# Performance work log

Hardware: AMD Instinct MI355X
Metric: run time of the kernel (lower is better)

The kernel has to match this reference:

```python
import jax, jax.numpy as jnp
import numpy as np

B, T, I, H, O = 64, 2048, 128, 256, 1

def setup_inputs() -> dict:
    key = jax.random.key(0)
    ks = jax.random.split(key, 7)
    s = 0.05
    return {
        "x": jax.random.normal(ks[0], (B, T, I), jnp.float32),
        "W_ih": jax.random.normal(ks[1], (3 * H, I), jnp.float32) * s,
        "W_hh": jax.random.normal(ks[2], (3 * H, H), jnp.float32) * s,
        "b_ih": jax.random.normal(ks[3], (3 * H,), jnp.float32) * s,
        "b_hh": jax.random.normal(ks[4], (3 * H,), jnp.float32) * s,
        "W_o": jax.random.normal(ks[5], (O, H), jnp.float32) * s,
        "b_o": jax.random.normal(ks[6], (O,), jnp.float32) * s,
    }

def _gru_scan(x, W_ih, W_hh, b_ih, b_hh):
    # Precompute input projections for all timesteps: [T, B, 3H]
    gi = jnp.einsum('bti,gi->tbg', x, W_ih) + b_ih
    Hd = W_hh.shape[1]

    def step(h, gi_t):
        gh = h @ W_hh.T + b_hh  # [B, 3H]
        i_r, i_z, i_n = jnp.split(gi_t, 3, axis=-1)
        h_r, h_z, h_n = jnp.split(gh, 3, axis=-1)
        r = jax.nn.sigmoid(i_r + h_r)
        z = jax.nn.sigmoid(i_z + h_z)
        n = jnp.tanh(i_n + r * h_n)
        h_new = (1.0 - z) * n + z * h
        return h_new, h_new

    h0 = jnp.zeros((x.shape[0], Hd), x.dtype)
    _, hs = jax.lax.scan(step, h0, gi)  # hs: [T, B, H]
    return hs

def reference(x, W_ih, W_hh, b_ih, b_hh, W_o, b_o):
    hs = _gru_scan(x, W_ih, W_hh, b_ih, b_hh)        # [T, B, H]
    outputs = jnp.einsum('tbh,oh->bto', hs, W_o) + b_o  # [B, T, O], identity nonlinearity
    hiddens = jnp.transpose(hs, (1, 0, 2))              # [B, T, H]
    return outputs, hiddens
```

## Files before the change

### kernel.cpp

```cpp
#include <hip/hip_runtime.h>
#include <hip/hip_bf16.h>

#define BB 64
#define TT 2048
#define II 128
#define HH 256
#define GG 768

typedef _Float16 h2 __attribute__((ext_vector_type(2)));
union U32H2 { unsigned int u; h2 h; };

static __device__ __forceinline__ float fdot2f(unsigned int w, h2 hv, float acc){
#if __has_builtin(__builtin_amdgcn_fdot2)
    U32H2 c; c.u = w;
    return __builtin_amdgcn_fdot2(c.h, hv, acc, false);
#else
    U32H2 c; c.u = w;
    return acc + (float)c.h.x * (float)hv.x + (float)c.h.y * (float)hv.y;
#endif
}

__global__ void conv_whh(const float* __restrict__ Whh, unsigned int* __restrict__ Wt){
    int idx = blockIdx.x * 256 + threadIdx.x;
    int kk = idx / GG;
    int g  = idx - kk * GG;
    float a = Whh[g * HH + 2*kk];
    float b = Whh[g * HH + 2*kk + 1];
    U32H2 c; c.h.x = (_Float16)a; c.h.y = (_Float16)b;
    Wt[idx] = c.u;
}

__global__ __launch_bounds__(256) void gi_gemm(const float* __restrict__ x,
                                               const float* __restrict__ Wih,
                                               const float* __restrict__ bih,
                                               _Float16* __restrict__ gi){
    __shared__ float xs [128 * 132];
    __shared__ float wsh[128 * 132];
    const int bt0 = blockIdx.x * 128;
    const int g0  = blockIdx.y * 128;
    const int tid = threadIdx.x;
    for (int i = tid; i < 128 * 128; i += 256){
        int r = i >> 7, c = i & 127;
        xs [c * 132 + r] = x  [(size_t)(bt0 + r) * II + c];
        wsh[c * 132 + r] = Wih[(size_t)(g0  + r) * II + c];
    }
    __syncthreads();
    const int ty = tid >> 4, tx = tid & 15;
    float acc[8][8] = {};
    for (int k = 0; k < 128; ++k){
        const float4 a0 = *(const float4*)&xs [k * 132 + ty * 8];
        const float4 a1 = *(const float4*)&xs [k * 132 + ty * 8 + 4];
        const float4 b0 = *(const float4*)&wsh[k * 132 + tx * 4];
        const float4 b1 = *(const float4*)&wsh[k * 132 + tx * 4 + 64];
        const float av[8] = {a0.x,a0.y,a0.z,a0.w,a1.x,a1.y,a1.z,a1.w};
        const float bv[8] = {b0.x,b0.y,b0.z,b0.w,b1.x,b1.y,b1.z,b1.w};
        #pragma unroll
        for (int ii = 0; ii < 8; ++ii)
            #pragma unroll
            for (int jj = 0; jj < 8; ++jj)
                acc[ii][jj] += av[ii] * bv[jj];
    }
    #pragma unroll
    for (int ii = 0; ii < 8; ++ii){
        const int bt = bt0 + ty * 8 + ii;
        _Float16* gp = gi + (size_t)bt * GG + g0;
        #pragma unroll
        for (int jj = 0; jj < 8; ++jj){
            int gl = (jj < 4) ? (tx * 4 + jj) : (64 + tx * 4 + (jj - 4));
            gp[gl] = (_Float16)(acc[ii][jj] + bih[g0 + gl]);
        }
    }
}

__global__ __launch_bounds__(512, 2) void gru_rec(
        const unsigned int* __restrict__ Wt,
        const _Float16* __restrict__ gi,
        const float* __restrict__ bhh,
        float* __restrict__ hid)
{
    const int b    = blockIdx.x;
    const int tid  = threadIdx.x;
    const int j    = tid & 255;
    const int half = tid >> 8;

    unsigned int Wr[64], Wz[64], Wn[64];
    {
        const unsigned int* Wb = Wt + half * 64 * GG;
        #pragma unroll
        for (int m = 0; m < 64; ++m){
            Wr[m] = Wb[m * GG + j];
            Wz[m] = Wb[m * GG + j + 256];
            Wn[m] = Wb[m * GG + j + 512];
        }
    }
    float br = 0.f, bz = 0.f, bn = 0.f;
    if (half == 0){ br = bhh[j]; bz = bhh[j + 256]; bn = bhh[j + 512]; }

    __shared__ __align__(16) _Float16 hps[256];
    __shared__ float pr[256], pz[256], pn[256];
    if (tid < 256) hps[tid] = (_Float16)0.f;

    float h_prev = 0.f;
    const _Float16* gib = gi + (size_t)b * TT * GG;
    float* hob = hid + (size_t)b * TT * HH;
    __syncthreads();

    for (int t = 0; t < TT; ++t){
        float gir = 0.f, giz = 0.f, gin = 0.f;
        if (half == 0){
            const _Float16* g3 = gib + (size_t)t * GG + j;
            gir = (float)g3[0]; giz = (float)g3[256]; gin = (float)g3[512];
        }
        float ar = br, az = bz, an = bn;
        const uint4* hv = ((const uint4*)hps) + half * 16;
        #pragma unroll
        for (int mm = 0; mm < 16; ++mm){
            union { uint4 v; h2 p[4]; } hh;
            hh.v = hv[mm];
            #pragma unroll
            for (int q = 0; q < 4; ++q){
                ar = fdot2f(Wr[4*mm + q], hh.p[q], ar);
                az = fdot2f(Wz[4*mm + q], hh.p[q], az);
                an = fdot2f(Wn[4*mm + q], hh.p[q], an);
            }
        }
        if (half == 1){ pr[j] = ar; pz[j] = az; pn[j] = an; }
        __syncthreads();
        if (half == 0){
            float ghr = ar + pr[j];
            float ghz = az + pz[j];
            float ghn = an + pn[j];
            float r = 1.f / (1.f + __expf(-(gir + ghr)));
            float z = 1.f / (1.f + __expf(-(giz + ghz)));
            float tin = gin + r * ghn;
            tin = fminf(15.f, fmaxf(-15.f, tin));
            float e2 = __expf(2.f * tin);
            float n = (e2 - 1.f) / (e2 + 1.f);
            float hn = (1.f - z) * n + z * h_prev;
            h_prev = hn;
            hob[(size_t)t * HH + j] = hn;
            hps[j] = (_Float16)hn;
        }
        __syncthreads();
    }
}

__global__ __launch_bounds__(256) void out_proj(const float* __restrict__ hid,
                                                const float* __restrict__ Wo,
                                                const float* __restrict__ bo,
                                                float* __restrict__ outp){
    const int w = threadIdx.x >> 6, l = threadIdx.x & 63;
    const size_t bt = (size_t)blockIdx.x * 4 + w;
    const float4 hv = ((const float4*)(hid + bt * HH))[l];
    const float4 wv = ((const float4*)Wo)[l];
    float s = hv.x*wv.x + hv.y*wv.y + hv.z*wv.z + hv.w*wv.w;
    #pragma unroll
    for (int off = 32; off > 0; off >>= 1) s += __shfl_down(s, off, 64);
    if (l == 0) outp[bt] = s + bo[0];
}

extern "C" void kernel_launch(void* const* d_in, const int* in_sizes, int n_in,
                              void* d_out, int out_size, void* d_ws, size_t ws_size,
                              hipStream_t stream) {
    const float* x   = (const float*)d_in[0];
    const float* Wih = (const float*)d_in[1];
    const float* Whh = (const float*)d_in[2];
    const float* bih = (const float*)d_in[3];
    const float* bhh = (const float*)d_in[4];
    const float* Wo  = (const float*)d_in[5];
    const float* bo  = (const float*)d_in[6];

    float* outputs = (float*)d_out;
    float* hiddens = (float*)d_out + (size_t)BB * TT;

    unsigned int* Wt = (unsigned int*)d_ws;
    _Float16* gi = (_Float16*)((char*)d_ws + 128 * GG * sizeof(unsigned int));

    conv_whh<<<dim3(98304 / 256), dim3(256), 0, stream>>>(Whh, Wt);
    gi_gemm <<<dim3((BB * TT) / 128, GG / 128), dim3(256), 0, stream>>>(x, Wih, bih, gi);
    gru_rec <<<dim3(BB), dim3(512), 0, stream>>>(Wt, gi, bhh, hiddens);
    out_proj<<<dim3((BB * TT) / 4), dim3(256), 0, stream>>>(hiddens, Wo, bo, outputs);
}
```

Before: 2.907 ms.

## Use MFMA for input projection and split GRU recurrence across four thread quarters

Replaces the FP32 shared-memory SGEMM for the input projection with an fp16 MFMA kernel that reads x directly and uses a pre-converted fp16 W_ih. The recurrent kernel now splits the hidden-dimension reduction across four 256-thread groups instead of two, so each thread holds half as many weight registers and does half the dot products per step. The partial sums are combined through shared memory by the first group. The aim is to shorten the serial per-timestep critical path and speed up the projection GEMM. The costs are an extra reduction pass, a larger block of 1024 threads, and lower precision in the input projection.

```diff
diff --git a/kernel.cpp b/kernel.cpp
--- a/kernel.cpp
+++ b/kernel.cpp
@@ -8,6 +8,8 @@
 #define GG 768
 
 typedef _Float16 h2 __attribute__((ext_vector_type(2)));
+typedef _Float16 half8 __attribute__((ext_vector_type(8)));
+typedef float f32x4 __attribute__((ext_vector_type(4)));
 union U32H2 { unsigned int u; h2 h; };
 
 static __device__ __forceinline__ float fdot2f(unsigned int w, h2 hv, float acc){
@@ -30,74 +32,73 @@
     Wt[idx] = c.u;
 }
 
-__global__ __launch_bounds__(256) void gi_gemm(const float* __restrict__ x,
-                                               const float* __restrict__ Wih,
+__global__ void conv_wih(const float* __restrict__ Wih, _Float16* __restrict__ Wh){
+    int idx = blockIdx.x * 256 + threadIdx.x;
+    Wh[idx] = (_Float16)Wih[idx];
+}
+
+__global__ __launch_bounds__(256) void gi_mfma(const float* __restrict__ x,
+                                               const _Float16* __restrict__ Wh,
                                                const float* __restrict__ bih,
                                                _Float16* __restrict__ gi){
-    __shared__ float xs [128 * 132];
-    __shared__ float wsh[128 * 132];
-    const int bt0 = blockIdx.x * 128;
-    const int g0  = blockIdx.y * 128;
-    const int tid = threadIdx.x;
-    for (int i = tid; i < 128 * 128; i += 256){
-        int r = i >> 7, c = i & 127;
-        xs [c * 132 + r] = x  [(size_t)(bt0 + r) * II + c];
-        wsh[c * 132 + r] = Wih[(size_t)(g0  + r) * II + c];
-    }
-    __syncthreads();
-    const int ty = tid >> 4, tx = tid & 15;
-    float acc[8][8] = {};
-    for (int k = 0; k < 128; ++k){
-        const float4 a0 = *(const float4*)&xs [k * 132 + ty * 8];
-        const float4 a1 = *(const float4*)&xs [k * 132 + ty * 8 + 4];
-        const float4 b0 = *(const float4*)&wsh[k * 132 + tx * 4];
-        const float4 b1 = *(const float4*)&wsh[k * 132 + tx * 4 + 64];
-        const float av[8] = {a0.x,a0.y,a0.z,a0.w,a1.x,a1.y,a1.z,a1.w};
-        const float bv[8] = {b0.x,b0.y,b0.z,b0.w,b1.x,b1.y,b1.z,b1.w};
+    const int wave = threadIdx.x >> 6;
+    const int lane = threadIdx.x & 63;
+    const int l16  = lane & 15, q = lane >> 4;
+    const int m    = blockIdx.x * 64 + wave * 16 + l16;
+    const int n0   = blockIdx.y * 64;
+    f32x4 acc[4] = {};
+    #pragma unroll
+    for (int s = 0; s < 4; ++s){
+        const float* xp = x + (size_t)m * II + s*32 + q*8;
+        float4 a0 = *(const float4*)xp;
+        float4 a1 = *(const float4*)(xp + 4);
+        half8 af = { (_Float16)a0.x,(_Float16)a0.y,(_Float16)a0.z,(_Float16)a0.w,
+                     (_Float16)a1.x,(_Float16)a1.y,(_Float16)a1.z,(_Float16)a1.w };
         #pragma unroll
-        for (int ii = 0; ii < 8; ++ii)
-            #pragma unroll
-            for (int jj = 0; jj < 8; ++jj)
-                acc[ii][jj] += av[ii] * bv[jj];
+        for (int t = 0; t < 4; ++t){
+            const _Float16* wp = Wh + (size_t)(n0 + t*16 + l16) * II + s*32 + q*8;
+            half8 bf = *(const half8*)wp;
+            acc[t] = __builtin_amdgcn_mfma_f32_16x16x32_f16(af, bf, acc[t], 0, 0, 0);
+        }
     }
     #pragma unroll
-    for (int ii = 0; ii < 8; ++ii){
-        const int bt = bt0 + ty * 8 + ii;
-        _Float16* gp = gi + (size_t)bt * GG + g0;
+    for (int t = 0; t < 4; ++t){
+        int n = n0 + t*16 + l16;
+        float bv = bih[n];
         #pragma unroll
-        for (int jj = 0; jj < 8; ++jj){
-            int gl = (jj < 4) ? (tx * 4 + jj) : (64 + tx * 4 + (jj - 4));
-            gp[gl] = (_Float16)(acc[ii][jj] + bih[g0 + gl]);
+        for (int r = 0; r < 4; ++r){
+            int row = blockIdx.x*64 + wave*16 + q*4 + r;
+            gi[(size_t)row * GG + n] = (_Float16)(acc[t][r] + bv);
         }
     }
 }
 
-__global__ __launch_bounds__(512, 2) void gru_rec(
+__global__ __launch_bounds__(1024) void gru_rec(
         const unsigned int* __restrict__ Wt,
         const _Float16* __restrict__ gi,
         const float* __restrict__ bhh,
         float* __restrict__ hid)
 {
-    const int b    = blockIdx.x;
-    const int tid  = threadIdx.x;
-    const int j    = tid & 255;
-    const int half = tid >> 8;
+    const int b   = blockIdx.x;
+    const int tid = threadIdx.x;
+    const int j   = tid & 255;
+    const int q   = tid >> 8;
 
-    unsigned int Wr[64], Wz[64], Wn[64];
+    unsigned int Wr[32], Wz[32], Wn[32];
     {
-        const unsigned int* Wb = Wt + half * 64 * GG;
+        const unsigned int* Wb = Wt + q * 32 * GG;
         #pragma unroll
-        for (int m = 0; m < 64; ++m){
+        for (int m = 0; m < 32; ++m){
             Wr[m] = Wb[m * GG + j];
             Wz[m] = Wb[m * GG + j + 256];
             Wn[m] = Wb[m * GG + j + 512];
         }
     }
     float br = 0.f, bz = 0.f, bn = 0.f;
-    if (half == 0){ br = bhh[j]; bz = bhh[j + 256]; bn = bhh[j + 512]; }
+    if (q == 0){ br = bhh[j]; bz = bhh[j + 256]; bn = bhh[j + 512]; }
 
     __shared__ __align__(16) _Float16 hps[256];
-    __shared__ float pr[256], pz[256], pn[256];
+    __shared__ float pbuf[3 * GG];
     if (tid < 256) hps[tid] = (_Float16)0.f;
 
     float h_prev = 0.f;
@@ -107,32 +108,35 @@
 
     for (int t = 0; t < TT; ++t){
         float gir = 0.f, giz = 0.f, gin = 0.f;
-        if (half == 0){
+        if (q == 0){
             const _Float16* g3 = gib + (size_t)t * GG + j;
             gir = (float)g3[0]; giz = (float)g3[256]; gin = (float)g3[512];
         }
         float ar = br, az = bz, an = bn;
-        const uint4* hv = ((const uint4*)hps) + half * 16;
+        const uint4* hv = ((const uint4*)hps) + q * 8;
         #pragma unroll
-        for (int mm = 0; mm < 16; ++mm){
+        for (int mm = 0; mm < 8; ++mm){
             union { uint4 v; h2 p[4]; } hh;
             hh.v = hv[mm];
             #pragma unroll
-            for (int q = 0; q < 4; ++q){
-                ar = fdot2f(Wr[4*mm + q], hh.p[q], ar);
-                az = fdot2f(Wz[4*mm + q], hh.p[q], az);
-                an = fdot2f(Wn[4*mm + q], hh.p[q], an);
+            for (int p = 0; p < 4; ++p){
+                ar = fdot2f(Wr[4*mm + p], hh.p[p], ar);
+                az = fdot2f(Wz[4*mm + p], hh.p[p], az);
+                an = fdot2f(Wn[4*mm + p], hh.p[p], an);
             }
         }
-        if (half == 1){ pr[j] = ar; pz[j] = az; pn[j] = an; }
+        if (q){
+            float* pb = pbuf + (q - 1) * GG;
+            pb[j] = ar; pb[j + 256] = az; pb[j + 512] = an;
+        }
         __syncthreads();
-        if (half == 0){
-            float ghr = ar + pr[j];
-            float ghz = az + pz[j];
-            float ghn = an + pn[j];
-            float r = 1.f / (1.f + __expf(-(gir + ghr)));
-            float z = 1.f / (1.f + __expf(-(giz + ghz)));
-            float tin = gin + r * ghn;
+        if (q == 0){
+            ar += pbuf[j]       + pbuf[GG + j]       + pbuf[2*GG + j];
+            az += pbuf[j + 256] + pbuf[GG + j + 256] + pbuf[2*GG + j + 256];
+            an += pbuf[j + 512] + pbuf[GG + j + 512] + pbuf[2*GG + j + 512];
+            float r = 1.f / (1.f + __expf(-(gir + ar)));
+            float z = 1.f / (1.f + __expf(-(giz + az)));
+            float tin = gin + r * an;
             tin = fminf(15.f, fmaxf(-15.f, tin));
             float e2 = __expf(2.f * tin);
             float n = (e2 - 1.f) / (e2 + 1.f);
@@ -174,10 +178,12 @@
     float* hiddens = (float*)d_out + (size_t)BB * TT;
 
     unsigned int* Wt = (unsigned int*)d_ws;
-    _Float16* gi = (_Float16*)((char*)d_ws + 128 * GG * sizeof(unsigned int));
+    _Float16* Wh = (_Float16*)((char*)d_ws + 128 * GG * sizeof(unsigned int));
+    _Float16* gi = (_Float16*)((char*)Wh + (size_t)GG * II * sizeof(_Float16));
 
     conv_whh<<<dim3(98304 / 256), dim3(256), 0, stream>>>(Whh, Wt);
-    gi_gemm <<<dim3((BB * TT) / 128, GG / 128), dim3(256), 0, stream>>>(x, Wih, bih, gi);
-    gru_rec <<<dim3(BB), dim3(512), 0, stream>>>(Wt, gi, bhh, hiddens);
+    conv_wih<<<dim3(98304 / 256), dim3(256), 0, stream>>>(Wih, Wh);
+    gi_mfma <<<dim3((BB * TT) / 64, GG / 64), dim3(256), 0, stream>>>(x, Wh, bih, gi);
+    gru_rec <<<dim3(BB), dim3(1024), 0, stream>>>(Wt, gi, bhh, hiddens);
     out_proj<<<dim3((BB * TT) / 4), dim3(256), 0, stream>>>(hiddens, Wo, bo, outputs);
 }
```

New measurement: 2.620 ms. 9.9% less time.
